# Kernel optimization log

Hardware: AMD Instinct MI355X
Metric: run time of the kernel (lower is better)

## Reference

```python
import jax, jax.numpy as jnp
import numpy as np

N = 262144          # nodes
E = N * 16          # edges (avg degree 16)
C_IN = 64
C_OUT = 64
GRID = 0.5          # voxel size
POS_EXTENT = 10.0   # pos in [0, 10)^3
NVOX_DIM = int(round(POS_EXTENT / GRID))  # 20
NVOX = NVOX_DIM ** 3                      # 8000 voxels
BN_EPS = 1e-5


def setup_inputs() -> dict:
    key = jax.random.key(0)
    k = jax.random.split(key, 5)
    x = jax.random.normal(k[0], (N, C_IN), dtype=jnp.float32)
    pos = jax.random.uniform(k[1], (N, 3), dtype=jnp.float32, minval=0.0, maxval=POS_EXTENT)
    edge_index = jax.random.randint(k[2], (2, E), 0, N, dtype=jnp.int32)
    W = jax.random.normal(k[3], (C_IN, C_OUT), dtype=jnp.float32) / np.float32(np.sqrt(C_IN))
    b = jnp.zeros((C_OUT,), jnp.float32)
    gamma = jnp.ones((C_OUT,), jnp.float32)
    beta = jnp.zeros((C_OUT,), jnp.float32)
    return {"x": x, "pos": pos, "edge_index": edge_index,
            "W": W, "b": b, "gamma": gamma, "beta": beta}


def reference(x, pos, edge_index, W, b, gamma, beta):
    # --- self.down: Linear -> BatchNorm1d (training-mode batch stats) -> ReLU ---
    h = x @ W + b                                   # [N, C_OUT]
    mean = jnp.mean(h, axis=0)
    var = jnp.mean(jnp.square(h - mean), axis=0)    # biased variance (torch BN)
    h = (h - mean) * jax.lax.rsqrt(var + BN_EPS) * gamma + beta
    h = jax.nn.relu(h)

    # --- max_pool_neighbor_x: scatter-max of neighbor features (self-loops added) ---
    row, col = edge_index[0], edge_index[1]
    pooled = jax.ops.segment_max(h[row], col, num_segments=N)  # [N, C_OUT]
    h = jnp.maximum(pooled, h)  # self-loop; also fixes -inf for isolated nodes

    # --- GridSampling: voxel-grid quantize + per-voxel mean of x and pos ---
    vid = jnp.clip(jnp.floor(pos / GRID).astype(jnp.int32), 0, NVOX_DIM - 1)  # [N,3]
    vox = (vid[:, 0] * NVOX_DIM + vid[:, 1]) * NVOX_DIM + vid[:, 2]           # [N]
    cnt = jax.ops.segment_sum(jnp.ones((N,), jnp.float32), vox, num_segments=NVOX)
    x_sum = jax.ops.segment_sum(h, vox, num_segments=NVOX)     # [NVOX, C_OUT]
    p_sum = jax.ops.segment_sum(pos, vox, num_segments=NVOX)   # [NVOX, 3]
    denom = jnp.maximum(cnt, 1.0)[:, None]
    x_out = x_sum / denom
    pos_out = p_sum / denom
    # concat features and positions of the downsampled graph: [NVOX, C_OUT+3]
    return jnp.concatenate([x_out, pos_out], axis=1)
```

## Files before the change

kernel.cpp:

```cpp
#include <hip/hip_runtime.h>
#include <hip/hip_fp16.h>

#define NVOX_DIM 20
#define NVOX 8000
#define BN_EPS 1e-5f

#define NBUCK 1024
#define BSHIFT 8
#define NODES_PER_BUCK 256
#define GEMM_BLOCKS 1024
#define ZERO_BLOCKS 64
#define CAP 5120

typedef _Float16 f16x8 __attribute__((ext_vector_type(8)));
typedef float f32x4 __attribute__((ext_vector_type(4)));

__device__ __forceinline__ unsigned short f2key(float v) {
    unsigned short hb = __half_as_ushort(__float2half(v));
    unsigned short m = (unsigned short)(0x8000u | (unsigned short)(-(int)(hb >> 15)));
    return (unsigned short)(hb ^ m);
}

__global__ __launch_bounds__(256) void k0_fused(const float* __restrict__ x,
                                                const float* __restrict__ W,
                                                const float* __restrict__ bias,
                                                unsigned short* __restrict__ h16,
                                                float* __restrict__ partials, int n16,
                                                float4* __restrict__ zero_zone,
                                                int zero_n4) {
    __shared__ float sW[4096];
    __shared__ float red[2][4][64];
    int t = threadIdx.x;

    if (blockIdx.x >= GEMM_BLOCKS) {
        int zb = blockIdx.x - GEMM_BLOCKS;
        float4 z = {0.f, 0.f, 0.f, 0.f};
        for (int i = zb * 256 + t; i < zero_n4; i += ZERO_BLOCKS * 256) zero_zone[i] = z;
        return;
    }

    for (int i = t; i < 4096; i += 256) sW[i] = W[i];
    __syncthreads();
    int lane = t & 63;
    int w = t >> 6;
    int l15 = lane & 15;
    int q = lane >> 4;

    f16x8 bf[4][2];
#pragma unroll
    for (int t4 = 0; t4 < 4; ++t4)
#pragma unroll
        for (int kb = 0; kb < 2; ++kb)
#pragma unroll
            for (int i = 0; i < 8; ++i)
                bf[t4][kb][i] = (_Float16)sW[(kb * 32 + q * 8 + i) * 64 + t4 * 16 + l15];
    float bv[4];
#pragma unroll
    for (int t4 = 0; t4 < 4; ++t4) bv[t4] = bias[t4 * 16 + l15];

    float s[4] = {0.f, 0.f, 0.f, 0.f}, s2[4] = {0.f, 0.f, 0.f, 0.f};

    for (int g = blockIdx.x * 4 + w; g < n16; g += GEMM_BLOCKS * 4) {
        int row0 = g * 16;
        const float* xp = x + (size_t)(row0 + l15) * 64 + q * 8;
        float4 xa = *(const float4*)(xp);
        float4 xb = *(const float4*)(xp + 4);
        float4 xc = *(const float4*)(xp + 32);
        float4 xd = *(const float4*)(xp + 36);
        f16x8 a0, a1;
        a0[0] = (_Float16)xa.x; a0[1] = (_Float16)xa.y; a0[2] = (_Float16)xa.z; a0[3] = (_Float16)xa.w;
        a0[4] = (_Float16)xb.x; a0[5] = (_Float16)xb.y; a0[6] = (_Float16)xb.z; a0[7] = (_Float16)xb.w;
        a1[0] = (_Float16)xc.x; a1[1] = (_Float16)xc.y; a1[2] = (_Float16)xc.z; a1[3] = (_Float16)xc.w;
        a1[4] = (_Float16)xd.x; a1[5] = (_Float16)xd.y; a1[6] = (_Float16)xd.z; a1[7] = (_Float16)xd.w;

#pragma unroll
        for (int t4 = 0; t4 < 4; ++t4) {
            f32x4 acc = {bv[t4], bv[t4], bv[t4], bv[t4]};
            acc = __builtin_amdgcn_mfma_f32_16x16x32_f16(a0, bf[t4][0], acc, 0, 0, 0);
            acc = __builtin_amdgcn_mfma_f32_16x16x32_f16(a1, bf[t4][1], acc, 0, 0, 0);
            s[t4] += acc[0] + acc[1] + acc[2] + acc[3];
            s2[t4] = fmaf(acc[0], acc[0], s2[t4]);
            s2[t4] = fmaf(acc[1], acc[1], s2[t4]);
            s2[t4] = fmaf(acc[2], acc[2], s2[t4]);
            s2[t4] = fmaf(acc[3], acc[3], s2[t4]);
#pragma unroll
            for (int r = 0; r < 4; ++r) {
                h16[(size_t)(row0 + q * 4 + r) * 64 + t4 * 16 + l15] = f2key(acc[r]);
            }
        }
    }

#pragma unroll
    for (int t4 = 0; t4 < 4; ++t4) {
        s[t4] += __shfl_xor(s[t4], 16, 64);
        s[t4] += __shfl_xor(s[t4], 32, 64);
        s2[t4] += __shfl_xor(s2[t4], 16, 64);
        s2[t4] += __shfl_xor(s2[t4], 32, 64);
    }
    if (lane < 16) {
#pragma unroll
        for (int t4 = 0; t4 < 4; ++t4) {
            red[0][w][t4 * 16 + lane] = s[t4];
            red[1][w][t4 * 16 + lane] = s2[t4];
        }
    }
    __syncthreads();
    if (t < 128) {
        int c = t & 63;
        int which = t >> 6;
        float v = red[which][0][c] + red[which][1][c] + red[which][2][c] + red[which][3][c];
        partials[(size_t)blockIdx.x * 128 + which * 64 + c] = v;
    }
}

__global__ __launch_bounds__(1024) void k3_finalize(const float* __restrict__ partials,
                                                    const float* __restrict__ gamma,
                                                    const float* __restrict__ beta,
                                                    float* __restrict__ stats2, float invN) {
    __shared__ float red[8][128];
    __shared__ float tot[128];
    int t = threadIdx.x;
    int c = t & 127;
    int g = t >> 7;
    float s = 0.f;
    for (int b = g; b < GEMM_BLOCKS; b += 8) s += partials[(size_t)b * 128 + c];
    red[g][c] = s;
    __syncthreads();
    if (t < 128) {
        float v = 0.f;
#pragma unroll
        for (int g2 = 0; g2 < 8; ++g2) v += red[g2][t];
        tot[t] = v;
    }
    __syncthreads();
    if (t < 64) {
        float mean = tot[t] * invN;
        float var = tot[64 + t] * invN - mean * mean;
        float sc = gamma[t] * rsqrtf(var + BN_EPS);
        stats2[t] = sc;
        stats2[64 + t] = beta[t] - mean * sc;
    }
}

__global__ __launch_bounds__(1024) void k_bin(const int* __restrict__ rows,
                                              const int* __restrict__ cols,
                                              int* __restrict__ cursor,
                                              unsigned int* __restrict__ pairs, int E) {
    __shared__ int lh[NBUCK];
    __shared__ int lpos[NBUCK];
    int t = threadIdx.x;
    lh[t] = 0;
    __syncthreads();
    int base = blockIdx.x * 16384 + t * 16;
    int r[16], c[16];
#pragma unroll
    for (int g4 = 0; g4 < 4; ++g4) {
        int e = base + g4 * 4;
        int4 r4 = *(const int4*)(rows + e);
        int4 c4 = *(const int4*)(cols + e);
        r[g4 * 4 + 0] = r4.x; c[g4 * 4 + 0] = c4.x;
        r[g4 * 4 + 1] = r4.y; c[g4 * 4 + 1] = c4.y;
        r[g4 * 4 + 2] = r4.z; c[g4 * 4 + 2] = c4.z;
        r[g4 * 4 + 3] = r4.w; c[g4 * 4 + 3] = c4.w;
    }
#pragma unroll
    for (int i = 0; i < 16; ++i) atomicAdd(&lh[c[i] >> BSHIFT], 1);
    __syncthreads();
    int res = atomicAdd(&cursor[t], lh[t]);
    lpos[t] = res;
    __syncthreads();
#pragma unroll
    for (int i = 0; i < 16; ++i) {
        int bkt = c[i] >> BSHIFT;
        int idx = atomicAdd(&lpos[bkt], 1);
        if (idx < CAP)
            pairs[(size_t)bkt * CAP + idx] =
                ((unsigned int)r[i] << 8) | (unsigned int)(c[i] & (NODES_PER_BUCK - 1));
    }
}

__global__ __launch_bounds__(1024) void k_pool(const unsigned int* __restrict__ pairs,
                                               const int* __restrict__ cursor,
                                               const unsigned short* __restrict__ h16,
                                               const float* __restrict__ pos,
                                               const float* __restrict__ stats2,
                                               float* __restrict__ xs,
                                               float* __restrict__ ps,
                                               float* __restrict__ cnt) {
    __shared__ unsigned int tile[NODES_PER_BUCK * 64];
    int b = blockIdx.x;
    int t = threadIdx.x;
    int lane = t & 63;
    int w = t >> 6;
    float scale = stats2[lane];
    float shift = stats2[64 + lane];

    const unsigned int* src = (const unsigned int*)(h16 + (size_t)b * (NODES_PER_BUCK * 64));
#pragma unroll
    for (int k = 0; k < 8; ++k) {
        int i = t + k * 1024;
        unsigned int u = src[i];
        tile[2 * i] = u & 0xFFFFu;
        tile[2 * i + 1] = u >> 16;
    }
    __syncthreads();

    int cntE = min(cursor[b], CAP);
    int start = b * CAP;
    int end = start + cntE;
    int chunk = (cntE + 15) >> 4;
    int cs = start + w * chunk;
    int ce = min(cs + chunk, end);
    for (int j0 = cs; j0 < ce; j0 += 64) {
        int lim = min(64, ce - j0);
        unsigned int pk = (lane < lim) ? pairs[j0 + lane] : 0u;
        int jj = 0;
        for (; jj + 16 <= lim; jj += 16) {
            unsigned int qv[16];
            unsigned short vv[16];
#pragma unroll
            for (int u = 0; u < 16; ++u)
                qv[u] = (unsigned int)__builtin_amdgcn_readlane((int)pk, jj + u);
#pragma unroll
            for (int u = 0; u < 16; ++u) vv[u] = h16[(size_t)(qv[u] >> 8) * 64 + lane];
#pragma unroll
            for (int u = 0; u < 16; ++u)
                atomicMax(&tile[((qv[u] & 255u) << 6) + lane], (unsigned int)vv[u]);
        }
        for (; jj < lim; ++jj) {
            unsigned int qq = (unsigned int)__builtin_amdgcn_readlane((int)pk, jj);
            unsigned int v = h16[(size_t)(qq >> 8) * 64 + lane];
            atomicMax(&tile[((qq & 255u) << 6) + lane], v);
        }
    }
    __syncthreads();

#pragma unroll
    for (int nl = 0; nl < NODES_PER_BUCK; nl += 16) {
        int node_l = nl + w;
        int c = (b << BSHIFT) + node_l;
        float px = pos[(size_t)c * 3 + 0];
        float py = pos[(size_t)c * 3 + 1];
        float pz = pos[(size_t)c * 3 + 2];
        int v0 = min(max((int)floorf(px * 2.f), 0), NVOX_DIM - 1);
        int v1 = min(max((int)floorf(py * 2.f), 0), NVOX_DIM - 1);
        int v2 = min(max((int)floorf(pz * 2.f), 0), NVOX_DIM - 1);
        int vox = (v0 * NVOX_DIM + v1) * NVOX_DIM + v2;
        unsigned int k = tile[(node_l << 6) + lane];
        unsigned short hb = (k & 0x8000u) ? (unsigned short)(k ^ 0x8000u)
                                          : (unsigned short)(0xFFFFu ^ k);
        __half_raw hr;
        hr.x = hb;
        float v = __half2float((__half)hr);
        float val = fmaxf(fmaf(v, scale, shift), 0.f);
        atomicAdd(&xs[(size_t)vox * 64 + lane], val);
        if (lane < 3) atomicAdd(&ps[vox * 3 + lane], lane == 0 ? px : (lane == 1 ? py : pz));
        if (lane == 0) atomicAdd(&cnt[vox], 1.f);
    }
}

__global__ __launch_bounds__(256) void k7_out(const float* __restrict__ xs,
                                              const float* __restrict__ ps,
                                              const float* __restrict__ cnt,
                                              float* __restrict__ out, int total) {
    int idx = blockIdx.x * blockDim.x + threadIdx.x;
    if (idx >= total) return;
    int v = idx / 67;
    int c = idx - v * 67;
    float d = fmaxf(cnt[v], 1.f);
    float val = (c < 64) ? xs[(size_t)v * 64 + c] : ps[v * 3 + (c - 64)];
    out[idx] = val / d;
}

extern "C" void kernel_launch(void* const* d_in, const int* in_sizes, int n_in,
                              void* d_out, int out_size, void* d_ws, size_t ws_size,
                              hipStream_t stream) {
    const float* x     = (const float*)d_in[0];
    const float* pos   = (const float*)d_in[1];
    const int*   ei    = (const int*)d_in[2];
    const float* W     = (const float*)d_in[3];
    const float* b     = (const float*)d_in[4];
    const float* gamma = (const float*)d_in[5];
    const float* beta  = (const float*)d_in[6];
    float* out = (float*)d_out;

    const int n = in_sizes[0] / 64;
    const int E = in_sizes[2] / 2;

    char* ws = (char*)d_ws;
    unsigned short* h16      = (unsigned short*)(ws + 0);
    unsigned int*   pairs    = (unsigned int*)(ws + 33554432);
    float*          partials = (float*)(ws + 54525952);
    float*          stats2   = (float*)(ws + 55050240);
    int*            cursor   = (int*)(ws + 55051264);
    float*          xs       = (float*)(ws + 55055360);
    float*          ps       = (float*)(ws + 57103360);
    float*          cnt      = (float*)(ws + 57199360);
    float4*         zero4    = (float4*)(ws + 55051264);
    const int zero_n4 = (57231360 - 55051264) / 16;

    k0_fused<<<GEMM_BLOCKS + ZERO_BLOCKS, 256, 0, stream>>>(x, W, b, h16, partials,
                                                            n >> 4, zero4, zero_n4);
    k3_finalize<<<1, 1024, 0, stream>>>(partials, gamma, beta, stats2, 1.0f / (float)n);
    k_bin<<<E / 16384, 1024, 0, stream>>>(ei, ei + E, cursor, pairs, E);
    k_pool<<<NBUCK, 1024, 0, stream>>>(pairs, cursor, h16, pos, stats2, xs, ps, cnt);
    k7_out<<<(out_size + 255) / 256, 256, 0, stream>>>(xs, ps, cnt, out, out_size);
}
```

Before: 347.6 us.

## Fuse edge binning into GEMM kernel as interleaved blocks

```diff
diff --git a/kernel.cpp b/kernel.cpp
--- a/kernel.cpp
+++ b/kernel.cpp
@@ -9,6 +9,7 @@
 #define BSHIFT 8
 #define NODES_PER_BUCK 256
 #define GEMM_BLOCKS 1024
+#define BIN_BLOCKS 1024
 #define ZERO_BLOCKS 64
 #define CAP 5120
 
@@ -19,6 +20,11 @@
     unsigned short hb = __half_as_ushort(__float2half(v));
     unsigned short m = (unsigned short)(0x8000u | (unsigned short)(-(int)(hb >> 15)));
     return (unsigned short)(hb ^ m);
+}
+
+__global__ __launch_bounds__(256) void k_zero_cursor(int* __restrict__ cursor) {
+    int i = blockIdx.x * 256 + threadIdx.x;
+    if (i < NBUCK) cursor[i] = 0;
 }
 
 __global__ __launch_bounds__(256) void k0_fused(const float* __restrict__ x,
@@ -26,19 +32,59 @@
                                                 const float* __restrict__ bias,
                                                 unsigned short* __restrict__ h16,
                                                 float* __restrict__ partials, int n16,
+                                                const int* __restrict__ rows,
+                                                const int* __restrict__ cols,
+                                                int* __restrict__ cursor,
+                                                unsigned int* __restrict__ pairs,
                                                 float4* __restrict__ zero_zone,
                                                 int zero_n4) {
     __shared__ float sW[4096];
     __shared__ float red[2][4][64];
+    __shared__ int lh[NBUCK];
+    __shared__ int lpos[NBUCK];
     int t = threadIdx.x;
-
-    if (blockIdx.x >= GEMM_BLOCKS) {
-        int zb = blockIdx.x - GEMM_BLOCKS;
+    int bid = blockIdx.x;
+
+    if (bid >= 2 * GEMM_BLOCKS) {
+        int zb = bid - 2 * GEMM_BLOCKS;
         float4 z = {0.f, 0.f, 0.f, 0.f};
         for (int i = zb * 256 + t; i < zero_n4; i += ZERO_BLOCKS * 256) zero_zone[i] = z;
         return;
     }
 
+    if (bid & 1) {
+        int bb = bid >> 1;
+        for (int j = t; j < NBUCK; j += 256) lh[j] = 0;
+        __syncthreads();
+        int base = bb * 4096 + t * 16;
+        int r[16], c[16];
+#pragma unroll
+        for (int g4 = 0; g4 < 4; ++g4) {
+            int e = base + g4 * 4;
+            int4 r4 = *(const int4*)(rows + e);
+            int4 c4 = *(const int4*)(cols + e);
+            r[g4 * 4 + 0] = r4.x; c[g4 * 4 + 0] = c4.x;
+            r[g4 * 4 + 1] = r4.y; c[g4 * 4 + 1] = c4.y;
+            r[g4 * 4 + 2] = r4.z; c[g4 * 4 + 2] = c4.z;
+            r[g4 * 4 + 3] = r4.w; c[g4 * 4 + 3] = c4.w;
+        }
+#pragma unroll
+        for (int i = 0; i < 16; ++i) atomicAdd(&lh[c[i] >> BSHIFT], 1);
+        __syncthreads();
+        for (int j = t; j < NBUCK; j += 256) lpos[j] = atomicAdd(&cursor[j], lh[j]);
+        __syncthreads();
+#pragma unroll
+        for (int i = 0; i < 16; ++i) {
+            int bkt = c[i] >> BSHIFT;
+            int idx = atomicAdd(&lpos[bkt], 1);
+            if (idx < CAP)
+                pairs[(size_t)bkt * CAP + idx] =
+                    ((unsigned int)r[i] << 8) | (unsigned int)(c[i] & (NODES_PER_BUCK - 1));
+        }
+        return;
+    }
+
+    int gb = bid >> 1;
     for (int i = t; i < 4096; i += 256) sW[i] = W[i];
     __syncthreads();
     int lane = t & 63;
@@ -60,7 +106,7 @@
 
     float s[4] = {0.f, 0.f, 0.f, 0.f}, s2[4] = {0.f, 0.f, 0.f, 0.f};
 
-    for (int g = blockIdx.x * 4 + w; g < n16; g += GEMM_BLOCKS * 4) {
+    for (int g = gb * 4 + w; g < n16; g += GEMM_BLOCKS * 4) {
         int row0 = g * 16;
         const float* xp = x + (size_t)(row0 + l15) * 64 + q * 8;
         float4 xa = *(const float4*)(xp);
@@ -109,7 +155,7 @@
         int c = t & 63;
         int which = t >> 6;
         float v = red[which][0][c] + red[which][1][c] + red[which][2][c] + red[which][3][c];
-        partials[(size_t)blockIdx.x * 128 + which * 64 + c] = v;
+        partials[(size_t)gb * 128 + which * 64 + c] = v;
     }
 }
 
@@ -139,43 +185,6 @@
         float sc = gamma[t] * rsqrtf(var + BN_EPS);
         stats2[t] = sc;
         stats2[64 + t] = beta[t] - mean * sc;
-    }
-}
-
-__global__ __launch_bounds__(1024) void k_bin(const int* __restrict__ rows,
-                                              const int* __restrict__ cols,
-                                              int* __restrict__ cursor,
-                                              unsigned int* __restrict__ pairs, int E) {
-    __shared__ int lh[NBUCK];
-    __shared__ int lpos[NBUCK];
-    int t = threadIdx.x;
-    lh[t] = 0;
-    __syncthreads();
-    int base = blockIdx.x * 16384 + t * 16;
-    int r[16], c[16];
-#pragma unroll
-    for (int g4 = 0; g4 < 4; ++g4) {
-        int e = base + g4 * 4;
-        int4 r4 = *(const int4*)(rows + e);
-        int4 c4 = *(const int4*)(cols + e);
-        r[g4 * 4 + 0] = r4.x; c[g4 * 4 + 0] = c4.x;
-        r[g4 * 4 + 1] = r4.y; c[g4 * 4 + 1] = c4.y;
-        r[g4 * 4 + 2] = r4.z; c[g4 * 4 + 2] = c4.z;
-        r[g4 * 4 + 3] = r4.w; c[g4 * 4 + 3] = c4.w;
-    }
-#pragma unroll
-    for (int i = 0; i < 16; ++i) atomicAdd(&lh[c[i] >> BSHIFT], 1);
-    __syncthreads();
-    int res = atomicAdd(&cursor[t], lh[t]);
-    lpos[t] = res;
-    __syncthreads();
-#pragma unroll
-    for (int i = 0; i < 16; ++i) {
-        int bkt = c[i] >> BSHIFT;
-        int idx = atomicAdd(&lpos[bkt], 1);
-        if (idx < CAP)
-            pairs[(size_t)bkt * CAP + idx] =
-                ((unsigned int)r[i] << 8) | (unsigned int)(c[i] & (NODES_PER_BUCK - 1));
     }
 }
 
@@ -296,13 +305,13 @@
     float*          xs       = (float*)(ws + 55055360);
     float*          ps       = (float*)(ws + 57103360);
     float*          cnt      = (float*)(ws + 57199360);
-    float4*         zero4    = (float4*)(ws + 55051264);
-    const int zero_n4 = (57231360 - 55051264) / 16;
-
-    k0_fused<<<GEMM_BLOCKS + ZERO_BLOCKS, 256, 0, stream>>>(x, W, b, h16, partials,
-                                                            n >> 4, zero4, zero_n4);
+    float4*         zero4    = (float4*)(ws + 55055360);
+    const int zero_n4 = (57231360 - 55055360) / 16;
+
+    k_zero_cursor<<<4, 256, 0, stream>>>(cursor);
+    k0_fused<<<2 * GEMM_BLOCKS + ZERO_BLOCKS, 256, 0, stream>>>(
+        x, W, b, h16, partials, n >> 4, ei, ei + E, cursor, pairs, zero4, zero_n4);
     k3_finalize<<<1, 1024, 0, stream>>>(partials, gamma, beta, stats2, 1.0f / (float)n);
-    k_bin<<<E / 16384, 1024, 0, stream>>>(ei, ei + E, cursor, pairs, E);
     k_pool<<<NBUCK, 1024, 0, stream>>>(pairs, cursor, h16, pos, stats2, xs, ps, cnt);
     k7_out<<<(out_size + 255) / 256, 256, 0, stream>>>(xs, ps, cnt, out, out_size);
 }
```

New measurement: 340.5 us. 2.0% less time.
